# Optimization experiments

Hardware: AMD Instinct MI355X
Metric: run time of the kernel (lower is better)

## Reference

```python
import jax, jax.numpy as jnp
import numpy as np

NSEQ, NRES, MSA_DIM, PAIR_DIM, NHEAD = 128, 256, 256, 128, 8
HEAD_DIM = MSA_DIM // NHEAD  # 32
EPS = 1e-5


def layer_norm(x, scale, bias):
    mu = jnp.mean(x, axis=-1, keepdims=True)
    var = jnp.var(x, axis=-1, keepdims=True)
    return (x - mu) * jax.lax.rsqrt(var + EPS) * scale + bias


def setup_inputs() -> dict:
    key = jax.random.key(0)
    ks = jax.random.split(key, 12)
    s = 0.02
    return {
        "msa_act": jax.random.normal(ks[0], (NSEQ, NRES, MSA_DIM), jnp.float32),
        "msa_mask": jnp.ones((NSEQ, NRES), jnp.float32),
        "pair_act": jax.random.normal(ks[1], (NRES, NRES, PAIR_DIM), jnp.float32),
        "qn_scale": jnp.ones((MSA_DIM,), jnp.float32),
        "qn_bias": jnp.zeros((MSA_DIM,), jnp.float32),
        "pn_scale": jnp.ones((PAIR_DIM,), jnp.float32),
        "pn_bias": jnp.zeros((PAIR_DIM,), jnp.float32),
        "feat2d_w": jax.random.normal(ks[2], (PAIR_DIM, NHEAD), jnp.float32) * s,
        "q_w": jax.random.normal(ks[3], (MSA_DIM, NHEAD, HEAD_DIM), jnp.float32) * s,
        "k_w": jax.random.normal(ks[4], (MSA_DIM, NHEAD, HEAD_DIM), jnp.float32) * s,
        "v_w": jax.random.normal(ks[5], (MSA_DIM, NHEAD, HEAD_DIM), jnp.float32) * s,
        "gating_w": jax.random.normal(ks[6], (MSA_DIM, NHEAD, HEAD_DIM), jnp.float32) * s,
        "gating_b": jnp.ones((NHEAD, HEAD_DIM), jnp.float32),
        "o_w": jax.random.normal(ks[7], (NHEAD, HEAD_DIM, MSA_DIM), jnp.float32) * s,
        "o_b": jnp.zeros((MSA_DIM,), jnp.float32),
    }


def reference(msa_act, msa_mask, pair_act, qn_scale, qn_bias, pn_scale, pn_bias,
              feat2d_w, q_w, k_w, v_w, gating_w, gating_b, o_w, o_b):
    # mask bias: [N_seq, 1, 1, N_res]
    mask_bias = (1e9 * (msa_mask - 1.0))[:, None, None, :]
    x = layer_norm(msa_act, qn_scale, qn_bias)            # [b, q, a]
    p = layer_norm(pair_act, pn_scale, pn_bias)           # [q, k, c]
    # pair -> per-head bias, permuted to [h, q, k]
    nonbatched_bias = jnp.einsum('qkc,ch->hqk', p, feat2d_w)
    q = jnp.einsum('bqa,ahc->bqhc', x, q_w) * (HEAD_DIM ** -0.5)
    k = jnp.einsum('bka,ahc->bkhc', x, k_w)
    v = jnp.einsum('bka,ahc->bkhc', x, v_w)
    logits = jnp.einsum('bqhc,bkhc->bhqk', q, k) + mask_bias + nonbatched_bias[None]
    weights = jax.nn.softmax(logits, axis=-1)
    weighted_avg = jnp.einsum('bhqk,bkhc->bqhc', weights, v)
    gate = jax.nn.sigmoid(jnp.einsum('bqa,ahc->bqhc', x, gating_w) + gating_b)
    out = jnp.einsum('bqhc,hco->bqo', weighted_avg * gate, o_w) + o_b
    return out
```

## Files before the change

### kernel.cpp

```cpp
#include <hip/hip_runtime.h>
#include <hip/hip_bf16.h>

typedef unsigned short u16;
typedef unsigned int u32;
typedef __attribute__((ext_vector_type(8))) short short8;
typedef __attribute__((ext_vector_type(4))) float f32x4;

__device__ __forceinline__ u16 f2b(float f) {
  u32 u = __builtin_bit_cast(u32, f);
  u += 0x7fffu + ((u >> 16) & 1u);
  return (u16)(u >> 16);
}
__device__ __forceinline__ u32 pkb(float a, float b) {
  u32 ua = __builtin_bit_cast(u32, a);
  u32 ub = __builtin_bit_cast(u32, b);
  ua += 0x7fffu + ((ua >> 16) & 1u);
  ub += 0x7fffu + ((ub >> 16) & 1u);
  return (ua >> 16) | (ub & 0xffff0000u);
}
__device__ __forceinline__ float b2f(u16 u) {
  u32 x = ((u32)u) << 16;
  return __builtin_bit_cast(float, x);
}
__device__ __forceinline__ void load_lds16(const u16* g, u16* l) {
  __builtin_amdgcn_global_load_lds(
      (const __attribute__((address_space(1))) void*)(uintptr_t)g,
      (__attribute__((address_space(3))) void*)(u32)(uintptr_t)l, 16, 0, 0);
}

#define LOG2E 1.4426950408889634f


__global__ __launch_bounds__(256) void k_msa(
    const float* __restrict__ msa, const float* __restrict__ qns,
    const float* __restrict__ qnb, u16* __restrict__ xb) {
  const int tid = threadIdx.x, blk = blockIdx.x;
  const int wid = tid >> 6, lane = tid & 63;
  const int r = lane >> 3, c = lane & 7;
  const int row = blk * 32 + wid * 8 + r;
  const float* src = msa + (size_t)row * 256 + c * 4;
  float4 v[8];
#pragma unroll
  for (int it = 0; it < 8; it++)
    v[it] = *(const float4*)(src + it * 32);
  float s = 0.f, s2 = 0.f;
#pragma unroll
  for (int it = 0; it < 8; it++) {
    s += v[it].x + v[it].y + v[it].z + v[it].w;
    s2 += v[it].x * v[it].x + v[it].y * v[it].y + v[it].z * v[it].z + v[it].w * v[it].w;
  }
#pragma unroll
  for (int m = 1; m < 8; m <<= 1) { s += __shfl_xor(s, m); s2 += __shfl_xor(s2, m); }
  const float mu = s * (1.f / 256.f);
  const float rs = rsqrtf(s2 * (1.f / 256.f) - mu * mu + 1e-5f);
  u16* dst = xb + (size_t)row * 256 + c * 4;
#pragma unroll
  for (int it = 0; it < 8; it++) {
    const int c0 = it * 32 + c * 4;
    const float4 scv = *(const float4*)(qns + c0);
    const float4 biv = *(const float4*)(qnb + c0);
    uint2 o;
    o.x = pkb((v[it].x - mu) * rs * scv.x + biv.x, (v[it].y - mu) * rs * scv.y + biv.y);
    o.y = pkb((v[it].z - mu) * rs * scv.z + biv.z, (v[it].w - mu) * rs * scv.w + biv.w);
    *(uint2*)(dst + it * 32) = o;
  }
}

__global__ __launch_bounds__(256) void k_tr(
    const float* __restrict__ qw, const float* __restrict__ kw,
    const float* __restrict__ vw, const float* __restrict__ gw,
    const float* __restrict__ ow, const float* __restrict__ pns,
    const float* __restrict__ pnb, const float* __restrict__ fw,
    u16* __restrict__ Wt, u16* __restrict__ OWt,
    float* __restrict__ wbuf, float* __restrict__ abuf) {
  const int tid = threadIdx.x;
  const int t = blockIdx.x;
  if (t == 80) {
    if (tid >= 64) return;
    const int lane = tid;
    const float4 f0a = *(const float4*)(fw + lane * 8);
    const float4 f1a = *(const float4*)(fw + lane * 8 + 4);
    const float4 f0b = *(const float4*)(fw + (lane + 64) * 8);
    const float4 f1b = *(const float4*)(fw + (lane + 64) * 8 + 4);
    const float sa = pns[lane] * LOG2E, sb = pns[lane + 64] * LOG2E;
    const float ba = pnb[lane] * LOG2E, bb = pnb[lane + 64] * LOG2E;
    float4 w0a = {f0a.x * sa, f0a.y * sa, f0a.z * sa, f0a.w * sa};
    float4 w1a = {f1a.x * sa, f1a.y * sa, f1a.z * sa, f1a.w * sa};
    float4 w0b = {f0b.x * sb, f0b.y * sb, f0b.z * sb, f0b.w * sb};
    float4 w1b = {f1b.x * sb, f1b.y * sb, f1b.z * sb, f1b.w * sb};
    *(float4*)(wbuf + lane * 8) = w0a;
    *(float4*)(wbuf + lane * 8 + 4) = w1a;
    *(float4*)(wbuf + (lane + 64) * 8) = w0b;
    *(float4*)(wbuf + (lane + 64) * 8 + 4) = w1b;
    float pa[8] = {w0a.x + w0b.x, w0a.y + w0b.y, w0a.z + w0b.z, w0a.w + w0b.w,
                   w1a.x + w1b.x, w1a.y + w1b.y, w1a.z + w1b.z, w1a.w + w1b.w};
    float pb[8] = {ba * f0a.x + bb * f0b.x, ba * f0a.y + bb * f0b.y,
                   ba * f0a.z + bb * f0b.z, ba * f0a.w + bb * f0b.w,
                   ba * f1a.x + bb * f1b.x, ba * f1a.y + bb * f1b.y,
                   ba * f1a.z + bb * f1b.z, ba * f1a.w + bb * f1b.w};
#pragma unroll
    for (int m = 1; m < 64; m <<= 1) {
#pragma unroll
      for (int h = 0; h < 8; h++) {
        pa[h] += __shfl_xor(pa[h], m);
        pb[h] += __shfl_xor(pb[h], m);
      }
    }
    if (lane == 0) {
      *(float4*)(abuf)      = float4{pa[0], pa[1], pa[2], pa[3]};
      *(float4*)(abuf + 4)  = float4{pa[4], pa[5], pa[6], pa[7]};
      *(float4*)(abuf + 8)  = float4{pb[0], pb[1], pb[2], pb[3]};
      *(float4*)(abuf + 12) = float4{pb[4], pb[5], pb[6], pb[7]};
    }
    return;
  }
  __shared__ u16 tlds[64 * 66];
  const int proj = t >> 4, tile = t & 15;
  const int tr = (tile >> 2) * 64, tc = (tile & 3) * 64;
  const float* src = proj == 0 ? qw : proj == 1 ? kw : proj == 2 ? vw
                      : proj == 3 ? gw : ow;
  u16* dst = proj < 4 ? (Wt + proj * 65536) : OWt;
  const float scale = proj == 0 ? 0.25503471881f : 1.f;
  {
    const int rl = tid >> 2, cg = (tid & 3) * 16;
    const float* sp = src + (size_t)(tr + rl) * 256 + tc + cg;
    float4 a0 = *(const float4*)(sp);
    float4 a1 = *(const float4*)(sp + 4);
    float4 a2 = *(const float4*)(sp + 8);
    float4 a3 = *(const float4*)(sp + 12);
    float xs[16] = {a0.x, a0.y, a0.z, a0.w, a1.x, a1.y, a1.z, a1.w,
                    a2.x, a2.y, a2.z, a2.w, a3.x, a3.y, a3.z, a3.w};
#pragma unroll
    for (int j = 0; j < 16; j++)
      tlds[(cg + j) * 66 + rl] = f2b(xs[j] * scale);
  }
  __syncthreads();
  {
    const int cl = tid >> 2, ag = (tid & 3) * 16;
    union { uint4 q[2]; u16 u[16]; } uu;
#pragma unroll
    for (int j = 0; j < 16; j++) uu.u[j] = tlds[cl * 66 + ag + j];
    u16* dp = dst + (size_t)(tc + cl) * 256 + tr + ag;
    *(uint4*)(dp) = uu.q[0];
    *(uint4*)(dp + 8) = uu.q[1];
  }
}

__global__ __launch_bounds__(256) void k_pair(
    const float* __restrict__ pair, const float* __restrict__ wbuf,
    const float* __restrict__ abuf, float* __restrict__ biasB) {
  __shared__ float Wpt[8][132];
  __shared__ float plds[512];
  const int tid = threadIdx.x, pb = blockIdx.x;
  const int ra = tid >> 3, hh = tid & 7;
  const int R0 = pb * 64 + ra;
  const float* p0 = pair + (size_t)R0 * 128 + hh * 4;
  const float* p1 = pair + (size_t)(R0 + 32) * 128 + hh * 4;
  float4 va[4], vb[4];
#pragma unroll
  for (int g = 0; g < 4; g++) va[g] = *(const float4*)(p0 + g * 32);
#pragma unroll
  for (int g = 0; g < 4; g++) vb[g] = *(const float4*)(p1 + g * 32);
  const int h = ((hh & 1) << 2) | (hh & 2) | ((hh >> 2) & 1);
  const float Ah = abuf[h], Bh = abuf[8 + h];
  {
    const float4 w = *(const float4*)(wbuf + tid * 4);
    const int ch = tid >> 1, hs = (tid & 1) * 4;
    Wpt[hs + 0][ch] = w.x; Wpt[hs + 1][ch] = w.y;
    Wpt[hs + 2][ch] = w.z; Wpt[hs + 3][ch] = w.w;
  }
  __syncthreads();
  float s1a = 0.f, s2a = 0.f, s1b = 0.f, s2b = 0.f;
#pragma unroll
  for (int g = 0; g < 4; g++) {
    s1a += va[g].x + va[g].y + va[g].z + va[g].w;
    s2a += va[g].x * va[g].x + va[g].y * va[g].y + va[g].z * va[g].z + va[g].w * va[g].w;
    s1b += vb[g].x + vb[g].y + vb[g].z + vb[g].w;
    s2b += vb[g].x * vb[g].x + vb[g].y * vb[g].y + vb[g].z * vb[g].z + vb[g].w * vb[g].w;
  }
  float dA[8] = {0.f, 0.f, 0.f, 0.f, 0.f, 0.f, 0.f, 0.f};
  float dB[8] = {0.f, 0.f, 0.f, 0.f, 0.f, 0.f, 0.f, 0.f};
#pragma unroll
  for (int g = 0; g < 4; g++) {
    const int cb = g * 32 + hh * 4;
#pragma unroll
    for (int hd = 0; hd < 8; hd++) {
      const float4 w = *(const float4*)(&Wpt[hd][cb]);
      dA[hd] += va[g].x * w.x + va[g].y * w.y + va[g].z * w.z + va[g].w * w.w;
      dB[hd] += vb[g].x * w.x + vb[g].y * w.y + vb[g].z * w.z + vb[g].w * w.w;
    }
  }
#pragma unroll
  for (int m = 1; m < 8; m <<= 1) {
    s1a += __shfl_xor(s1a, m); s2a += __shfl_xor(s2a, m);
    s1b += __shfl_xor(s1b, m); s2b += __shfl_xor(s2b, m);
  }
  const float muA = s1a * (1.f / 128.f);
  const float rA = rsqrtf(s2a * (1.f / 128.f) - muA * muA + 1e-5f);
  const float muB = s1b * (1.f / 128.f);
  const float rB = rsqrtf(s2b * (1.f / 128.f) - muB * muB + 1e-5f);
  float a0, a1, a2, a3, b0, b1, b2, b3;
  {
    const bool hi = (hh & 1) != 0;
    a0 = (hi ? dA[4] : dA[0]) + __shfl_xor(hi ? dA[0] : dA[4], 1);
    a1 = (hi ? dA[5] : dA[1]) + __shfl_xor(hi ? dA[1] : dA[5], 1);
    a2 = (hi ? dA[6] : dA[2]) + __shfl_xor(hi ? dA[2] : dA[6], 1);
    a3 = (hi ? dA[7] : dA[3]) + __shfl_xor(hi ? dA[3] : dA[7], 1);
    b0 = (hi ? dB[4] : dB[0]) + __shfl_xor(hi ? dB[0] : dB[4], 1);
    b1 = (hi ? dB[5] : dB[1]) + __shfl_xor(hi ? dB[1] : dB[5], 1);
    b2 = (hi ? dB[6] : dB[2]) + __shfl_xor(hi ? dB[2] : dB[6], 1);
    b3 = (hi ? dB[7] : dB[3]) + __shfl_xor(hi ? dB[3] : dB[7], 1);
  }
  {
    const bool hi = (hh & 2) != 0;
    const float ta0 = __shfl_xor(hi ? a0 : a2, 2);
    const float ta1 = __shfl_xor(hi ? a1 : a3, 2);
    const float tb0 = __shfl_xor(hi ? b0 : b2, 2);
    const float tb1 = __shfl_xor(hi ? b1 : b3, 2);
    a0 = (hi ? a2 : a0) + ta0;
    a1 = (hi ? a3 : a1) + ta1;
    b0 = (hi ? b2 : b0) + tb0;
    b1 = (hi ? b3 : b1) + tb1;
  }
  {
    const bool hi = (hh & 4) != 0;
    const float ta = __shfl_xor(hi ? a0 : a1, 4);
    const float tb = __shfl_xor(hi ? b0 : b1, 4);
    a0 = (hi ? a1 : a0) + ta;
    b0 = (hi ? b1 : b0) + tb;
  }
  const float vA = rA * (a0 - muA * Ah) + Bh;
  const float vB = rB * (b0 - muB * Ah) + Bh;
  const int slA = ((ra & 15) << 2) | ((ra >> 4) & 3);
  const int kb = ra + 32;
  const int slB = ((kb & 15) << 2) | ((kb >> 4) & 3);
  plds[h * 64 + slA] = vA;
  plds[h * 64 + slB] = vB;
  __syncthreads();
  const int q = (pb * 64) >> 8, g = pb & 3;
  const int j = tid * 2;
  *(float2*)(biasB + (j >> 6) * 65536 + q * 256 + g * 64 + (j & 63)) =
      *(const float2*)(plds + j);
}

template <bool OUT_BF16>
__global__ __launch_bounds__(256) void k_gemm(
    const u16* __restrict__ A, const u16* __restrict__ Bt,
    void* __restrict__ out, const float* __restrict__ obias, const int N) {
  __shared__ u16 As[128 * 32];
  __shared__ u16 Bs[128 * 32];
  const int tid = threadIdx.x, wid = tid >> 6, lane = tid & 63;
  const int quad = lane >> 4, l16 = lane & 15;
  const int wm = (wid >> 1) * 64, wn = (wid & 1) * 64;
  const int bm = blockIdx.x, bn = blockIdx.y;
  const int r0 = wid * 16 + (lane >> 2);
  const int kc = (lane & 3) * 8;
  const u16* gA0 = A + (size_t)(bm * 128 + r0) * 256 + kc;
  const u16* gA1 = A + (size_t)(bm * 128 + 64 + r0) * 256 + kc;
  const u16* gB0 = Bt + (size_t)(bn * 128 + r0) * 256 + kc;
  const u16* gB1 = Bt + (size_t)(bn * 128 + 64 + r0) * 256 + kc;
  u16* lA0 = As + wid * 512;
  u16* lA1 = As + 2048 + wid * 512;
  u16* lB0 = Bs + wid * 512;
  u16* lB1 = Bs + 2048 + wid * 512;
  f32x4 acc[4][4];
#pragma unroll
  for (int i = 0; i < 4; i++)
#pragma unroll
    for (int j = 0; j < 4; j++) acc[i][j] = f32x4{0.f, 0.f, 0.f, 0.f};
  for (int k0 = 0; k0 < 256; k0 += 32) {
    __syncthreads();
    load_lds16(gA0 + k0, lA0);
    load_lds16(gA1 + k0, lA1);
    load_lds16(gB0 + k0, lB0);
    load_lds16(gB1 + k0, lB1);
    __syncthreads();
    short8 af[4], bf[4];
#pragma unroll
    for (int i = 0; i < 4; i++)
      af[i] = *(const short8*)(As + (wm + i * 16 + l16) * 32 + quad * 8);
#pragma unroll
    for (int j = 0; j < 4; j++)
      bf[j] = *(const short8*)(Bs + (wn + j * 16 + l16) * 32 + quad * 8);
#pragma unroll
    for (int i = 0; i < 4; i++)
#pragma unroll
      for (int j = 0; j < 4; j++)
        acc[i][j] = __builtin_amdgcn_mfma_f32_16x16x32_bf16(af[i], bf[j], acc[i][j], 0, 0, 0);
  }
#pragma unroll
  for (int i = 0; i < 4; i++)
#pragma unroll
    for (int j = 0; j < 4; j++)
#pragma unroll
      for (int r = 0; r < 4; r++) {
        const int gm = bm * 128 + wm + i * 16 + quad * 4 + r;
        const int gn = bn * 128 + wn + j * 16 + l16;
        const float v = acc[i][j][r];
        if (OUT_BF16) ((u16*)out)[(size_t)gm * N + gn] = f2b(v);
        else ((float*)out)[(size_t)gm * N + gn] = v + obias[gn];
      }
}

__global__ __launch_bounds__(512, 4) void k_attn(
    const u16* __restrict__ Y, const float* __restrict__ biasB,
    const float* __restrict__ mask, const float* __restrict__ gb,
    u16* __restrict__ Z) {
  __shared__ u16 KsPs[9216];
  __shared__ u16 Vt[32 * 264];
  const int b = blockIdx.x, h = blockIdx.y, qh = blockIdx.z;
  const int tid = threadIdx.x, w = tid >> 6, lane = tid & 63;
  const int quad = lane >> 4, l16 = lane & 15;
  const int q0 = qh * 128 + w * 16;
  const u16* Yb = Y + (size_t)b * 256 * 1024;
  {
    const int kr = w * 32 + (lane >> 2), kc = (lane & 3) * 8;
    load_lds16(Yb + (size_t)kr * 1024 + 256 + h * 32 + kc, KsPs + (w * 32) * 32);
    load_lds16(Yb + (size_t)(kr + 16) * 1024 + 256 + h * 32 + kc, KsPs + (w * 32 + 16) * 32);
  }
  {
    const int slot = tid & 255, c0 = (tid >> 8) * 16;
    const int kv = ((slot >> 6) << 6) + ((slot & 3) << 4) + ((slot >> 2) & 15);
    const u16* src = Yb + (size_t)kv * 1024 + 512 + h * 32 + c0;
    union { uint4 q[2]; u16 u[16]; } uu;
    uu.q[0] = *(const uint4*)(src);
    uu.q[1] = *(const uint4*)(src + 8);
#pragma unroll
    for (int j = 0; j < 16; j++) Vt[(c0 + j) * 264 + slot] = uu.u[j];
  }
  const short8 aq = *(const short8*)(Yb + (size_t)(q0 + l16) * 1024 + h * 32 + quad * 8);
  float maskv[16];
#pragma unroll
  for (int ni = 0; ni < 16; ni++)
    maskv[ni] = 1.4426950409e9f * (mask[b * 256 + ni * 16 + l16] - 1.f);
  __syncthreads();
  f32x4 S[16];
#pragma unroll
  for (int ni = 0; ni < 16; ni++) S[ni] = f32x4{0.f, 0.f, 0.f, 0.f};
#pragma unroll
  for (int ni = 0; ni < 16; ni++) {
    const short8 bk = *(const short8*)(KsPs + (ni * 16 + l16) * 32 + quad * 8);
    S[ni] = __builtin_amdgcn_mfma_f32_16x16x32_bf16(aq, bk, S[ni], 0, 0, 0);
  }
  float li[4];
#pragma unroll
  for (int r = 0; r < 4; r++) {
    const int qg = q0 + quad * 4 + r;
    const float* bb = biasB + (h << 16) + (qg << 8) + l16 * 4;
    const float4 b0 = *(const float4*)(bb);
    const float4 b1 = *(const float4*)(bb + 64);
    const float4 b2 = *(const float4*)(bb + 128);
    const float4 b3 = *(const float4*)(bb + 192);
    const float bv[16] = {b0.x, b0.y, b0.z, b0.w, b1.x, b1.y, b1.z, b1.w,
                          b2.x, b2.y, b2.z, b2.w, b3.x, b3.y, b3.z, b3.w};
    float l = 0.f;
#pragma unroll
    for (int ni = 0; ni < 16; ni++) {
      const float p = __builtin_amdgcn_exp2f(S[ni][r] + bv[ni] + maskv[ni]);
      S[ni][r] = p;
      l += p;
    }
#pragma unroll
    for (int d = 1; d < 16; d <<= 1) l += __shfl_xor(l, d);
    li[r] = __builtin_amdgcn_rcpf(l);
  }
  __syncthreads();
  f32x4 O[2];
  O[0] = f32x4{0.f, 0.f, 0.f, 0.f};
  O[1] = f32x4{0.f, 0.f, 0.f, 0.f};
  u16* Pw = KsPs + w * 1152;
#pragma unroll
  for (int Q = 0; Q < 4; Q++) {
#pragma unroll
    for (int r = 0; r < 4; r++) {
      uint2 wv;
      wv.x = pkb(S[Q * 4 + 0][r], S[Q * 4 + 1][r]);
      wv.y = pkb(S[Q * 4 + 2][r], S[Q * 4 + 3][r]);
      *(uint2*)(Pw + (quad * 4 + r) * 72 + l16 * 4) = wv;
    }
#pragma unroll
    for (int ks = 0; ks < 2; ks++) {
      const short8 ap = *(const short8*)(Pw + l16 * 72 + ks * 32 + quad * 8);
#pragma unroll
      for (int nj = 0; nj < 2; nj++) {
        const short8 bv = *(const short8*)(Vt + (nj * 16 + l16) * 264 + Q * 64 + ks * 32 + quad * 8);
        O[nj] = __builtin_amdgcn_mfma_f32_16x16x32_bf16(ap, bv, O[nj], 0, 0, 0);
      }
    }
  }
  const float* gbh = gb + h * 32;
#pragma unroll
  for (int nj = 0; nj < 2; nj++)
#pragma unroll
    for (int r = 0; r < 4; r++) {
      const int qg = q0 + quad * 4 + r;
      const int c = nj * 16 + l16;
      const float wa = O[nj][r] * li[r];
      const float gv = b2f(Yb[(size_t)qg * 1024 + 768 + h * 32 + c]) + gbh[c];
      const float gate = __builtin_amdgcn_rcpf(1.f + __expf(-gv));
      Pw[(quad * 4 + r) * 40 + c] = f2b(wa * gate);
    }
  {
    const int qr = lane >> 2, cc = (lane & 3) * 8;
    const uint4 zv = *(const uint4*)(Pw + qr * 40 + cc);
    *(uint4*)(Z + ((size_t)(b * 256 + q0 + qr)) * 256 + h * 32 + cc) = zv;
  }
}

extern "C" void kernel_launch(void* const* d_in, const int* in_sizes, int n_in,
                              void* d_out, int out_size, void* d_ws, size_t ws_size,
                              hipStream_t stream) {
  const float* msa  = (const float*)d_in[0];
  const float* mask = (const float*)d_in[1];
  const float* pair = (const float*)d_in[2];
  const float* qns  = (const float*)d_in[3];
  const float* qnb  = (const float*)d_in[4];
  const float* pns  = (const float*)d_in[5];
  const float* pnb  = (const float*)d_in[6];
  const float* f2w  = (const float*)d_in[7];
  const float* qw   = (const float*)d_in[8];
  const float* kw   = (const float*)d_in[9];
  const float* vw   = (const float*)d_in[10];
  const float* gw   = (const float*)d_in[11];
  const float* gbp  = (const float*)d_in[12];
  const float* ow   = (const float*)d_in[13];
  const float* ob   = (const float*)d_in[14];
  float* out = (float*)d_out;
  char* ws = (char*)d_ws;
  u16*   xb    = (u16*)(ws);
  u16*   Wt    = (u16*)(ws + 16777216);
  u16*   OWt   = (u16*)(ws + 17301504);
  float* biasB = (float*)(ws + 17432576);
  u16*   Y     = (u16*)(ws + 19529728);
  u16*   Z     = (u16*)(ws + 86638592);
  float* wbuf  = (float*)(ws + 86638592);
  float* abuf  = wbuf + 1024;

  k_msa<<<1024, 256, 0, stream>>>(msa, qns, qnb, xb);
  k_tr<<<81, 256, 0, stream>>>(qw, kw, vw, gw, ow, pns, pnb, f2w,
                               Wt, OWt, wbuf, abuf);
  k_pair<<<1024, 256, 0, stream>>>(pair, wbuf, abuf, biasB);
  k_gemm<true><<<dim3(256, 8), 256, 0, stream>>>(xb, Wt, (void*)Y, nullptr, 1024);
  k_attn<<<dim3(128, 8, 2), 512, 0, stream>>>(Y, biasB, mask, gbp, Z);
  k_gemm<false><<<dim3(256, 2), 256, 0, stream>>>(Z, OWt, (void*)out, ob, 256);
}
```

Baseline: 218.3 us.

## Merge msa layernorm, pair bias and weight transpose into one prep kernel

Combines the three preprocessing kernels (msa layernorm, weight transpose, pair layernorm+bias projection) into a single launch whose block index selects the role. This removes the k_tr→k_pair dependency by computing the pair layernorm explicitly per element instead of relying on precomputed folded scale/bias sums. The aim is to cut two launches and the serialization between small kernels. The trade-off is more per-element work and LDS in the pair path. A shared LDS footprint and a launch_bounds occupancy hint apply to all block roles.

Result: faster. 212.1 us (-2.8%).

```diff
diff --git a/kernel.cpp b/kernel.cpp
--- a/kernel.cpp
+++ b/kernel.cpp
@@ -31,216 +31,184 @@
 #define LOG2E 1.4426950408889634f
 
 
-__global__ __launch_bounds__(256) void k_msa(
+__global__ __launch_bounds__(256, 2) void k_prep(
     const float* __restrict__ msa, const float* __restrict__ qns,
-    const float* __restrict__ qnb, u16* __restrict__ xb) {
+    const float* __restrict__ qnb, const float* __restrict__ pair,
+    const float* __restrict__ pns, const float* __restrict__ pnb,
+    const float* __restrict__ fw, const float* __restrict__ qw,
+    const float* __restrict__ kw, const float* __restrict__ vw,
+    const float* __restrict__ gw, const float* __restrict__ ow,
+    u16* __restrict__ xb, float* __restrict__ biasB,
+    u16* __restrict__ Wt, u16* __restrict__ OWt) {
+  __shared__ float Fpt[8][132];
+  __shared__ float plds[512];
+  __shared__ u16 tlds[64 * 66];
   const int tid = threadIdx.x, blk = blockIdx.x;
-  const int wid = tid >> 6, lane = tid & 63;
-  const int r = lane >> 3, c = lane & 7;
-  const int row = blk * 32 + wid * 8 + r;
-  const float* src = msa + (size_t)row * 256 + c * 4;
-  float4 v[8];
-#pragma unroll
-  for (int it = 0; it < 8; it++)
-    v[it] = *(const float4*)(src + it * 32);
-  float s = 0.f, s2 = 0.f;
-#pragma unroll
-  for (int it = 0; it < 8; it++) {
-    s += v[it].x + v[it].y + v[it].z + v[it].w;
-    s2 += v[it].x * v[it].x + v[it].y * v[it].y + v[it].z * v[it].z + v[it].w * v[it].w;
-  }
-#pragma unroll
-  for (int m = 1; m < 8; m <<= 1) { s += __shfl_xor(s, m); s2 += __shfl_xor(s2, m); }
-  const float mu = s * (1.f / 256.f);
-  const float rs = rsqrtf(s2 * (1.f / 256.f) - mu * mu + 1e-5f);
-  u16* dst = xb + (size_t)row * 256 + c * 4;
-#pragma unroll
-  for (int it = 0; it < 8; it++) {
-    const int c0 = it * 32 + c * 4;
-    const float4 scv = *(const float4*)(qns + c0);
-    const float4 biv = *(const float4*)(qnb + c0);
-    uint2 o;
-    o.x = pkb((v[it].x - mu) * rs * scv.x + biv.x, (v[it].y - mu) * rs * scv.y + biv.y);
-    o.y = pkb((v[it].z - mu) * rs * scv.z + biv.z, (v[it].w - mu) * rs * scv.w + biv.w);
-    *(uint2*)(dst + it * 32) = o;
-  }
-}
-
-__global__ __launch_bounds__(256) void k_tr(
-    const float* __restrict__ qw, const float* __restrict__ kw,
-    const float* __restrict__ vw, const float* __restrict__ gw,
-    const float* __restrict__ ow, const float* __restrict__ pns,
-    const float* __restrict__ pnb, const float* __restrict__ fw,
-    u16* __restrict__ Wt, u16* __restrict__ OWt,
-    float* __restrict__ wbuf, float* __restrict__ abuf) {
-  const int tid = threadIdx.x;
-  const int t = blockIdx.x;
-  if (t == 80) {
-    if (tid >= 64) return;
-    const int lane = tid;
-    const float4 f0a = *(const float4*)(fw + lane * 8);
-    const float4 f1a = *(const float4*)(fw + lane * 8 + 4);
-    const float4 f0b = *(const float4*)(fw + (lane + 64) * 8);
-    const float4 f1b = *(const float4*)(fw + (lane + 64) * 8 + 4);
-    const float sa = pns[lane] * LOG2E, sb = pns[lane + 64] * LOG2E;
-    const float ba = pnb[lane] * LOG2E, bb = pnb[lane + 64] * LOG2E;
-    float4 w0a = {f0a.x * sa, f0a.y * sa, f0a.z * sa, f0a.w * sa};
-    float4 w1a = {f1a.x * sa, f1a.y * sa, f1a.z * sa, f1a.w * sa};
-    float4 w0b = {f0b.x * sb, f0b.y * sb, f0b.z * sb, f0b.w * sb};
-    float4 w1b = {f1b.x * sb, f1b.y * sb, f1b.z * sb, f1b.w * sb};
-    *(float4*)(wbuf + lane * 8) = w0a;
-    *(float4*)(wbuf + lane * 8 + 4) = w1a;
-    *(float4*)(wbuf + (lane + 64) * 8) = w0b;
-    *(float4*)(wbuf + (lane + 64) * 8 + 4) = w1b;
-    float pa[8] = {w0a.x + w0b.x, w0a.y + w0b.y, w0a.z + w0b.z, w0a.w + w0b.w,
-                   w1a.x + w1b.x, w1a.y + w1b.y, w1a.z + w1b.z, w1a.w + w1b.w};
-    float pb[8] = {ba * f0a.x + bb * f0b.x, ba * f0a.y + bb * f0b.y,
-                   ba * f0a.z + bb * f0b.z, ba * f0a.w + bb * f0b.w,
-                   ba * f1a.x + bb * f1b.x, ba * f1a.y + bb * f1b.y,
-                   ba * f1a.z + bb * f1b.z, ba * f1a.w + bb * f1b.w};
-#pragma unroll
-    for (int m = 1; m < 64; m <<= 1) {
-#pragma unroll
-      for (int h = 0; h < 8; h++) {
-        pa[h] += __shfl_xor(pa[h], m);
-        pb[h] += __shfl_xor(pb[h], m);
+  if (blk < 1024) {
+    const int wid = tid >> 6, lane = tid & 63;
+    const int r = lane >> 3, c = lane & 7;
+    const int row = blk * 32 + wid * 8 + r;
+    const float* src = msa + (size_t)row * 256 + c * 4;
+    float4 v[8];
+#pragma unroll
+    for (int it = 0; it < 8; it++)
+      v[it] = *(const float4*)(src + it * 32);
+    float s = 0.f, s2 = 0.f;
+#pragma unroll
+    for (int it = 0; it < 8; it++) {
+      s += v[it].x + v[it].y + v[it].z + v[it].w;
+      s2 += v[it].x * v[it].x + v[it].y * v[it].y + v[it].z * v[it].z + v[it].w * v[it].w;
+    }
+#pragma unroll
+    for (int m = 1; m < 8; m <<= 1) { s += __shfl_xor(s, m); s2 += __shfl_xor(s2, m); }
+    const float mu = s * (1.f / 256.f);
+    const float rs = rsqrtf(s2 * (1.f / 256.f) - mu * mu + 1e-5f);
+    u16* dst = xb + (size_t)row * 256 + c * 4;
+#pragma unroll
+    for (int it = 0; it < 8; it++) {
+      const int c0 = it * 32 + c * 4;
+      const float4 scv = *(const float4*)(qns + c0);
+      const float4 biv = *(const float4*)(qnb + c0);
+      uint2 o;
+      o.x = pkb((v[it].x - mu) * rs * scv.x + biv.x, (v[it].y - mu) * rs * scv.y + biv.y);
+      o.y = pkb((v[it].z - mu) * rs * scv.z + biv.z, (v[it].w - mu) * rs * scv.w + biv.w);
+      *(uint2*)(dst + it * 32) = o;
+    }
+  } else if (blk < 2048) {
+    const int pb = blk - 1024;
+    const int ra = tid >> 3, hh = tid & 7;
+    const int R0 = pb * 64 + ra;
+    const float* p0 = pair + (size_t)R0 * 128 + hh * 4;
+    const float* p1 = pair + (size_t)(R0 + 32) * 128 + hh * 4;
+    float4 va[4], vb[4];
+#pragma unroll
+    for (int g = 0; g < 4; g++) va[g] = *(const float4*)(p0 + g * 32);
+#pragma unroll
+    for (int g = 0; g < 4; g++) vb[g] = *(const float4*)(p1 + g * 32);
+    float4 sc[4], bi[4];
+#pragma unroll
+    for (int g = 0; g < 4; g++) {
+      sc[g] = *(const float4*)(pns + g * 32 + hh * 4);
+      bi[g] = *(const float4*)(pnb + g * 32 + hh * 4);
+    }
+    const int h = ((hh & 1) << 2) | (hh & 2) | ((hh >> 2) & 1);
+    {
+      const float4 w = *(const float4*)(fw + tid * 4);
+      const int ch = tid >> 1, hs = (tid & 1) * 4;
+      Fpt[hs + 0][ch] = w.x * LOG2E; Fpt[hs + 1][ch] = w.y * LOG2E;
+      Fpt[hs + 2][ch] = w.z * LOG2E; Fpt[hs + 3][ch] = w.w * LOG2E;
+    }
+    __syncthreads();
+    float s1a = 0.f, s2a = 0.f, s1b = 0.f, s2b = 0.f;
+#pragma unroll
+    for (int g = 0; g < 4; g++) {
+      s1a += va[g].x + va[g].y + va[g].z + va[g].w;
+      s2a += va[g].x * va[g].x + va[g].y * va[g].y + va[g].z * va[g].z + va[g].w * va[g].w;
+      s1b += vb[g].x + vb[g].y + vb[g].z + vb[g].w;
+      s2b += vb[g].x * vb[g].x + vb[g].y * vb[g].y + vb[g].z * vb[g].z + vb[g].w * vb[g].w;
+    }
+#pragma unroll
+    for (int m = 1; m < 8; m <<= 1) {
+      s1a += __shfl_xor(s1a, m); s2a += __shfl_xor(s2a, m);
+      s1b += __shfl_xor(s1b, m); s2b += __shfl_xor(s2b, m);
+    }
+    const float muA = s1a * (1.f / 128.f);
+    const float rA = rsqrtf(s2a * (1.f / 128.f) - muA * muA + 1e-5f);
+    const float muB = s1b * (1.f / 128.f);
+    const float rB = rsqrtf(s2b * (1.f / 128.f) - muB * muB + 1e-5f);
+    float dA[8] = {0.f, 0.f, 0.f, 0.f, 0.f, 0.f, 0.f, 0.f};
+    float dB[8] = {0.f, 0.f, 0.f, 0.f, 0.f, 0.f, 0.f, 0.f};
+#pragma unroll
+    for (int g = 0; g < 4; g++) {
+      const int cb = g * 32 + hh * 4;
+      float4 xa, xbv;
+      xa.x = (va[g].x - muA) * rA * sc[g].x + bi[g].x;
+      xa.y = (va[g].y - muA) * rA * sc[g].y + bi[g].y;
+      xa.z = (va[g].z - muA) * rA * sc[g].z + bi[g].z;
+      xa.w = (va[g].w - muA) * rA * sc[g].w + bi[g].w;
+      xbv.x = (vb[g].x - muB) * rB * sc[g].x + bi[g].x;
+      xbv.y = (vb[g].y - muB) * rB * sc[g].y + bi[g].y;
+      xbv.z = (vb[g].z - muB) * rB * sc[g].z + bi[g].z;
+      xbv.w = (vb[g].w - muB) * rB * sc[g].w + bi[g].w;
+#pragma unroll
+      for (int hd = 0; hd < 8; hd++) {
+        const float4 w = *(const float4*)(&Fpt[hd][cb]);
+        dA[hd] += xa.x * w.x + xa.y * w.y + xa.z * w.z + xa.w * w.w;
+        dB[hd] += xbv.x * w.x + xbv.y * w.y + xbv.z * w.z + xbv.w * w.w;
       }
     }
-    if (lane == 0) {
-      *(float4*)(abuf)      = float4{pa[0], pa[1], pa[2], pa[3]};
-      *(float4*)(abuf + 4)  = float4{pa[4], pa[5], pa[6], pa[7]};
-      *(float4*)(abuf + 8)  = float4{pb[0], pb[1], pb[2], pb[3]};
-      *(float4*)(abuf + 12) = float4{pb[4], pb[5], pb[6], pb[7]};
-    }
-    return;
-  }
-  __shared__ u16 tlds[64 * 66];
-  const int proj = t >> 4, tile = t & 15;
-  const int tr = (tile >> 2) * 64, tc = (tile & 3) * 64;
-  const float* src = proj == 0 ? qw : proj == 1 ? kw : proj == 2 ? vw
-                      : proj == 3 ? gw : ow;
-  u16* dst = proj < 4 ? (Wt + proj * 65536) : OWt;
-  const float scale = proj == 0 ? 0.25503471881f : 1.f;
-  {
-    const int rl = tid >> 2, cg = (tid & 3) * 16;
-    const float* sp = src + (size_t)(tr + rl) * 256 + tc + cg;
-    float4 a0 = *(const float4*)(sp);
-    float4 a1 = *(const float4*)(sp + 4);
-    float4 a2 = *(const float4*)(sp + 8);
-    float4 a3 = *(const float4*)(sp + 12);
-    float xs[16] = {a0.x, a0.y, a0.z, a0.w, a1.x, a1.y, a1.z, a1.w,
-                    a2.x, a2.y, a2.z, a2.w, a3.x, a3.y, a3.z, a3.w};
-#pragma unroll
-    for (int j = 0; j < 16; j++)
-      tlds[(cg + j) * 66 + rl] = f2b(xs[j] * scale);
-  }
-  __syncthreads();
-  {
-    const int cl = tid >> 2, ag = (tid & 3) * 16;
-    union { uint4 q[2]; u16 u[16]; } uu;
-#pragma unroll
-    for (int j = 0; j < 16; j++) uu.u[j] = tlds[cl * 66 + ag + j];
-    u16* dp = dst + (size_t)(tc + cl) * 256 + tr + ag;
-    *(uint4*)(dp) = uu.q[0];
-    *(uint4*)(dp + 8) = uu.q[1];
-  }
-}
-
-__global__ __launch_bounds__(256) void k_pair(
-    const float* __restrict__ pair, const float* __restrict__ wbuf,
-    const float* __restrict__ abuf, float* __restrict__ biasB) {
-  __shared__ float Wpt[8][132];
-  __shared__ float plds[512];
-  const int tid = threadIdx.x, pb = blockIdx.x;
-  const int ra = tid >> 3, hh = tid & 7;
-  const int R0 = pb * 64 + ra;
-  const float* p0 = pair + (size_t)R0 * 128 + hh * 4;
-  const float* p1 = pair + (size_t)(R0 + 32) * 128 + hh * 4;
-  float4 va[4], vb[4];
-#pragma unroll
-  for (int g = 0; g < 4; g++) va[g] = *(const float4*)(p0 + g * 32);
-#pragma unroll
-  for (int g = 0; g < 4; g++) vb[g] = *(const float4*)(p1 + g * 32);
-  const int h = ((hh & 1) << 2) | (hh & 2) | ((hh >> 2) & 1);
-  const float Ah = abuf[h], Bh = abuf[8 + h];
-  {
-    const float4 w = *(const float4*)(wbuf + tid * 4);
-    const int ch = tid >> 1, hs = (tid & 1) * 4;
-    Wpt[hs + 0][ch] = w.x; Wpt[hs + 1][ch] = w.y;
-    Wpt[hs + 2][ch] = w.z; Wpt[hs + 3][ch] = w.w;
-  }
-  __syncthreads();
-  float s1a = 0.f, s2a = 0.f, s1b = 0.f, s2b = 0.f;
-#pragma unroll
-  for (int g = 0; g < 4; g++) {
-    s1a += va[g].x + va[g].y + va[g].z + va[g].w;
-    s2a += va[g].x * va[g].x + va[g].y * va[g].y + va[g].z * va[g].z + va[g].w * va[g].w;
-    s1b += vb[g].x + vb[g].y + vb[g].z + vb[g].w;
-    s2b += vb[g].x * vb[g].x + vb[g].y * vb[g].y + vb[g].z * vb[g].z + vb[g].w * vb[g].w;
-  }
-  float dA[8] = {0.f, 0.f, 0.f, 0.f, 0.f, 0.f, 0.f, 0.f};
-  float dB[8] = {0.f, 0.f, 0.f, 0.f, 0.f, 0.f, 0.f, 0.f};
-#pragma unroll
-  for (int g = 0; g < 4; g++) {
-    const int cb = g * 32 + hh * 4;
-#pragma unroll
-    for (int hd = 0; hd < 8; hd++) {
-      const float4 w = *(const float4*)(&Wpt[hd][cb]);
-      dA[hd] += va[g].x * w.x + va[g].y * w.y + va[g].z * w.z + va[g].w * w.w;
-      dB[hd] += vb[g].x * w.x + vb[g].y * w.y + vb[g].z * w.z + vb[g].w * w.w;
-    }
-  }
-#pragma unroll
-  for (int m = 1; m < 8; m <<= 1) {
-    s1a += __shfl_xor(s1a, m); s2a += __shfl_xor(s2a, m);
-    s1b += __shfl_xor(s1b, m); s2b += __shfl_xor(s2b, m);
-  }
-  const float muA = s1a * (1.f / 128.f);
-  const float rA = rsqrtf(s2a * (1.f / 128.f) - muA * muA + 1e-5f);
-  const float muB = s1b * (1.f / 128.f);
-  const float rB = rsqrtf(s2b * (1.f / 128.f) - muB * muB + 1e-5f);
-  float a0, a1, a2, a3, b0, b1, b2, b3;
-  {
-    const bool hi = (hh & 1) != 0;
-    a0 = (hi ? dA[4] : dA[0]) + __shfl_xor(hi ? dA[0] : dA[4], 1);
-    a1 = (hi ? dA[5] : dA[1]) + __shfl_xor(hi ? dA[1] : dA[5], 1);
-    a2 = (hi ? dA[6] : dA[2]) + __shfl_xor(hi ? dA[2] : dA[6], 1);
-    a3 = (hi ? dA[7] : dA[3]) + __shfl_xor(hi ? dA[3] : dA[7], 1);
-    b0 = (hi ? dB[4] : dB[0]) + __shfl_xor(hi ? dB[0] : dB[4], 1);
-    b1 = (hi ? dB[5] : dB[1]) + __shfl_xor(hi ? dB[1] : dB[5], 1);
-    b2 = (hi ? dB[6] : dB[2]) + __shfl_xor(hi ? dB[2] : dB[6], 1);
-    b3 = (hi ? dB[7] : dB[3]) + __shfl_xor(hi ? dB[3] : dB[7], 1);
-  }
-  {
-    const bool hi = (hh & 2) != 0;
-    const float ta0 = __shfl_xor(hi ? a0 : a2, 2);
-    const float ta1 = __shfl_xor(hi ? a1 : a3, 2);
-    const float tb0 = __shfl_xor(hi ? b0 : b2, 2);
-    const float tb1 = __shfl_xor(hi ? b1 : b3, 2);
-    a0 = (hi ? a2 : a0) + ta0;
-    a1 = (hi ? a3 : a1) + ta1;
-    b0 = (hi ? b2 : b0) + tb0;
-    b1 = (hi ? b3 : b1) + tb1;
-  }
-  {
-    const bool hi = (hh & 4) != 0;
-    const float ta = __shfl_xor(hi ? a0 : a1, 4);
-    const float tb = __shfl_xor(hi ? b0 : b1, 4);
-    a0 = (hi ? a1 : a0) + ta;
-    b0 = (hi ? b1 : b0) + tb;
-  }
-  const float vA = rA * (a0 - muA * Ah) + Bh;
-  const float vB = rB * (b0 - muB * Ah) + Bh;
-  const int slA = ((ra & 15) << 2) | ((ra >> 4) & 3);
-  const int kb = ra + 32;
-  const int slB = ((kb & 15) << 2) | ((kb >> 4) & 3);
-  plds[h * 64 + slA] = vA;
-  plds[h * 64 + slB] = vB;
-  __syncthreads();
-  const int q = (pb * 64) >> 8, g = pb & 3;
-  const int j = tid * 2;
-  *(float2*)(biasB + (j >> 6) * 65536 + q * 256 + g * 64 + (j & 63)) =
-      *(const float2*)(plds + j);
+    float a0, a1, a2, a3, b0, b1, b2, b3;
+    {
+      const bool hi = (hh & 1) != 0;
+      a0 = (hi ? dA[4] : dA[0]) + __shfl_xor(hi ? dA[0] : dA[4], 1);
+      a1 = (hi ? dA[5] : dA[1]) + __shfl_xor(hi ? dA[1] : dA[5], 1);
+      a2 = (hi ? dA[6] : dA[2]) + __shfl_xor(hi ? dA[2] : dA[6], 1);
+      a3 = (hi ? dA[7] : dA[3]) + __shfl_xor(hi ? dA[3] : dA[7], 1);
+      b0 = (hi ? dB[4] : dB[0]) + __shfl_xor(hi ? dB[0] : dB[4], 1);
+      b1 = (hi ? dB[5] : dB[1]) + __shfl_xor(hi ? dB[1] : dB[5], 1);
+      b2 = (hi ? dB[6] : dB[2]) + __shfl_xor(hi ? dB[2] : dB[6], 1);
+      b3 = (hi ? dB[7] : dB[3]) + __shfl_xor(hi ? dB[3] : dB[7], 1);
+    }
+    {
+      const bool hi = (hh & 2) != 0;
+      const float ta0 = __shfl_xor(hi ? a0 : a2, 2);
+      const float ta1 = __shfl_xor(hi ? a1 : a3, 2);
+      const float tb0 = __shfl_xor(hi ? b0 : b2, 2);
+      const float tb1 = __shfl_xor(hi ? b1 : b3, 2);
+      a0 = (hi ? a2 : a0) + ta0;
+      a1 = (hi ? a3 : a1) + ta1;
+      b0 = (hi ? b2 : b0) + tb0;
+      b1 = (hi ? b3 : b1) + tb1;
+    }
+    {
+      const bool hi = (hh & 4) != 0;
+      const float ta = __shfl_xor(hi ? a0 : a1, 4);
+      const float tb = __shfl_xor(hi ? b0 : b1, 4);
+      a0 = (hi ? a1 : a0) + ta;
+      b0 = (hi ? b1 : b0) + tb;
+    }
+    const int slA = ((ra & 15) << 2) | ((ra >> 4) & 3);
+    const int kb = ra + 32;
+    const int slB = ((kb & 15) << 2) | ((kb >> 4) & 3);
+    plds[h * 64 + slA] = a0;
+    plds[h * 64 + slB] = b0;
+    __syncthreads();
+    const int q = (pb * 64) >> 8, g = pb & 3;
+    const int j = tid * 2;
+    *(float2*)(biasB + (j >> 6) * 65536 + q * 256 + g * 64 + (j & 63)) =
+        *(const float2*)(plds + j);
+  } else {
+    const int t = blk - 2048;
+    const int proj = t >> 4, tile = t & 15;
+    const int tr = (tile >> 2) * 64, tc = (tile & 3) * 64;
+    const float* src = proj == 0 ? qw : proj == 1 ? kw : proj == 2 ? vw
+                        : proj == 3 ? gw : ow;
+    u16* dst = proj < 4 ? (Wt + proj * 65536) : OWt;
+    const float scale = proj == 0 ? 0.25503471881f : 1.f;
+    {
+      const int rl = tid >> 2, cg = (tid & 3) * 16;
+      const float* sp = src + (size_t)(tr + rl) * 256 + tc + cg;
+      float4 a0 = *(const float4*)(sp);
+      float4 a1 = *(const float4*)(sp + 4);
+      float4 a2 = *(const float4*)(sp + 8);
+      float4 a3 = *(const float4*)(sp + 12);
+      float xs[16] = {a0.x, a0.y, a0.z, a0.w, a1.x, a1.y, a1.z, a1.w,
+                      a2.x, a2.y, a2.z, a2.w, a3.x, a3.y, a3.z, a3.w};
+#pragma unroll
+      for (int j = 0; j < 16; j++)
+        tlds[(cg + j) * 66 + rl] = f2b(xs[j] * scale);
+    }
+    __syncthreads();
+    {
+      const int cl = tid >> 2, ag = (tid & 3) * 16;
+      union { uint4 q[2]; u16 u[16]; } uu;
+#pragma unroll
+      for (int j = 0; j < 16; j++) uu.u[j] = tlds[cl * 66 + ag + j];
+      u16* dp = dst + (size_t)(tc + cl) * 256 + tr + ag;
+      *(uint4*)(dp) = uu.q[0];
+      *(uint4*)(dp + 8) = uu.q[1];
+    }
+  }
 }
 
 template <bool OUT_BF16>
@@ -433,13 +401,9 @@
   float* biasB = (float*)(ws + 17432576);
   u16*   Y     = (u16*)(ws + 19529728);
   u16*   Z     = (u16*)(ws + 86638592);
-  float* wbuf  = (float*)(ws + 86638592);
-  float* abuf  = wbuf + 1024;
-
-  k_msa<<<1024, 256, 0, stream>>>(msa, qns, qnb, xb);
-  k_tr<<<81, 256, 0, stream>>>(qw, kw, vw, gw, ow, pns, pnb, f2w,
-                               Wt, OWt, wbuf, abuf);
-  k_pair<<<1024, 256, 0, stream>>>(pair, wbuf, abuf, biasB);
+
+  k_prep<<<2128, 256, 0, stream>>>(msa, qns, qnb, pair, pns, pnb, f2w,
+                                   qw, kw, vw, gw, ow, xb, biasB, Wt, OWt);
   k_gemm<true><<<dim3(256, 8), 256, 0, stream>>>(xb, Wt, (void*)Y, nullptr, 1024);
   k_attn<<<dim3(128, 8, 2), 512, 0, stream>>>(Y, biasB, mask, gbp, Z);
   k_gemm<false><<<dim3(256, 2), 256, 0, stream>>>(Z, OWt, (void*)out, ob, 256);
```
